# Kernel tuning notes

Measured on AMD Instinct MI355X. Metric: run time of the kernel, lower is better.

## Reference

```python
import jax, jax.numpy as jnp
import numpy as np

N = 100000   # nodes
E = 1000000  # edges (before self-loops)
G = 64       # graphs in batch
IN, HID, OUT = 128, 64, 1


def setup_inputs() -> dict:
    key = jax.random.key(0)
    ks = jax.random.split(key, 24)
    inp = {
        "x": jax.random.normal(ks[0], (N, IN), jnp.float32),
        "adj": jax.random.randint(ks[1], (2, E), 0, N, jnp.int32),
        "batch": jnp.sort(jax.random.randint(ks[2], (N,), 0, G, jnp.int32)),
    }
    i = 3
    dims = [(IN, HID), (HID, HID), (HID, HID)]
    for l, (di, do) in enumerate(dims, start=1):
        inp[f"W{l}"] = jax.random.normal(ks[i], (di, do), jnp.float32) * (1.0 / np.sqrt(di)); i += 1
        inp[f"a_src{l}"] = jax.random.normal(ks[i], (do,), jnp.float32) * 0.1; i += 1
        inp[f"a_dst{l}"] = jax.random.normal(ks[i], (do,), jnp.float32) * 0.1; i += 1
        inp[f"b{l}"] = jnp.zeros((do,), jnp.float32); i += 1
    inp["linnews_W"] = jax.random.normal(ks[i], (IN, HID), jnp.float32) * (1.0 / np.sqrt(IN)); i += 1
    inp["linnews_b"] = jnp.zeros((HID,), jnp.float32)
    inp["lin0_W"] = jax.random.normal(ks[i], (HID, HID), jnp.float32) * (1.0 / np.sqrt(HID)); i += 1
    inp["lin0_b"] = jnp.zeros((HID,), jnp.float32)
    inp["lin1_W"] = jax.random.normal(ks[i], (2 * HID, OUT), jnp.float32) * (1.0 / np.sqrt(2 * HID)); i += 1
    inp["lin1_b"] = jnp.zeros((OUT,), jnp.float32)
    return inp


def _gat_layer(x, src, dst, W, a_src, a_dst, b):
    # PyG GATConv, heads=1, self-loops already appended to (src, dst).
    h = x @ W                                        # [N, HID]
    e = (h @ a_src)[src] + (h @ a_dst)[dst]          # [E'] edge scores
    e = jax.nn.leaky_relu(e, 0.2)
    # segment softmax over incoming edges of each dst node
    m = jax.ops.segment_max(e, dst, num_segments=N)
    num = jnp.exp(e - m[dst])
    den = jax.ops.segment_sum(num, dst, num_segments=N)
    coef = num / (den[dst] + 1e-16)                  # [E']
    out = jax.ops.segment_sum(coef[:, None] * h[src], dst, num_segments=N)
    return out + b


def reference(x, adj, batch, W1, a_src1, a_dst1, b1, W2, a_src2, a_dst2, b2,
              W3, a_src3, a_dst3, b3, linnews_W, linnews_b, lin0_W, lin0_b,
              lin1_W, lin1_b):
    loop = jnp.arange(N, dtype=adj.dtype)
    src = jnp.concatenate([adj[0], loop])
    dst = jnp.concatenate([adj[1], loop])

    h = jax.nn.relu(_gat_layer(x, src, dst, W1, a_src1, a_dst1, b1))
    h = jax.nn.relu(_gat_layer(h, src, dst, W2, a_src2, a_dst2, b2))
    h = jax.nn.relu(_gat_layer(h, src, dst, W3, a_src3, a_dst3, b3))

    # global max pool per graph
    h = jax.ops.segment_max(h, batch, num_segments=G)        # [G, HID]
    h = jax.nn.relu(h @ lin0_W + lin0_b)

    # root node of each graph = first index with that batch id
    root = jax.ops.segment_min(jnp.arange(N), batch, num_segments=G)  # [G]
    news = jax.nn.relu(x[root] @ linnews_W + linnews_b)      # [G, HID]

    out = jnp.concatenate([h, news], axis=-1) @ lin1_W + lin1_b
    return jax.nn.sigmoid(out)                               # [G, 1]
```

## Files before the change

kernel.cpp:

```cpp
#include <hip/hip_runtime.h>
#include <hip/hip_fp16.h>
#include <cstdint>

#define THREADS 256
#define NBLK 64
#define BPAD 512
#define LINBLK 640

typedef _Float16 half8 __attribute__((ext_vector_type(8)));
typedef float v4f __attribute__((ext_vector_type(4)));

__global__ void init_kernel(float* pool, int* root, int G) {
  int i = blockIdx.x * blockDim.x + threadIdx.x;
  if (i < G * 64) pool[i] = 0.0f;
  if (i < G) root[i] = 0x7fffffff;
}

__global__ __launch_bounds__(256) void hist_kernel(const int* __restrict__ dst_e,
                                                   int* __restrict__ hist, int E, int chunk) {
  __shared__ int hcnt[BPAD];
  int t = threadIdx.x, blk = blockIdx.x;
  for (int i = t; i < BPAD; i += 256) hcnt[i] = 0;
  __syncthreads();
  int s = blk * chunk, e = s + chunk;
  if (e > E) e = E;
  for (int i = s + t; i < e; i += 256) atomicAdd(&hcnt[dst_e[i] >> 8], 1);
  __syncthreads();
  for (int b = t; b < BPAD; b += 256) hist[b * NBLK + blk] = hcnt[b];
}

__global__ __launch_bounds__(256) void hscan_kernel(int* __restrict__ hist) {
  __shared__ int part[256];
  const int PER = (BPAD * NBLK) / 256;
  int t = threadIdx.x;
  int base = t * PER;
  int sum = 0;
  for (int k = 0; k < PER; k++) sum += hist[base + k];
  part[t] = sum;
  __syncthreads();
  int own = sum;
  for (int off = 1; off < 256; off <<= 1) {
    int v = (t >= off) ? part[t - off] : 0;
    __syncthreads();
    part[t] += v;
    __syncthreads();
  }
  int run = part[t] - own;
  for (int k = 0; k < PER; k++) {
    int h = hist[base + k];
    hist[base + k] = run;
    run += h;
  }
}

__global__ __launch_bounds__(256) void scatter_kernel(const int* __restrict__ src_e,
                                                      const int* __restrict__ dst_e,
                                                      const int* __restrict__ hist,
                                                      unsigned int* __restrict__ ebuf,
                                                      int E, int chunk) {
  __shared__ int cur[BPAD];
  int t = threadIdx.x, blk = blockIdx.x;
  for (int b = t; b < BPAD; b += 256) cur[b] = hist[b * NBLK + blk];
  __syncthreads();
  int s = blk * chunk, e = s + chunk;
  if (e > E) e = E;
  for (int i = s + t; i < e; i += 256) {
    int d = dst_e[i];
    unsigned int sv = (unsigned int)src_e[i];
    int slot = atomicAdd(&cur[d >> 8], 1);
    ebuf[slot] = (sv << 8) | (unsigned int)(d & 255);
  }
}

__global__ __launch_bounds__(256) void build_kernel(const unsigned int* __restrict__ ebuf,
                                                    const int* __restrict__ hist,
                                                    int* __restrict__ row_start,
                                                    int* __restrict__ csr_src,
                                                    unsigned char* __restrict__ dst8,
                                                    int N, int E) {
  __shared__ int counts[256];
  __shared__ int sc[256];
  __shared__ int curw[256];
  int t = threadIdx.x, b = blockIdx.x;
  int nbase = b * 256;
  int ebase = hist[b * NBLK];
  int eend = hist[(b + 1) * NBLK];
  counts[t] = 0;
  __syncthreads();
  int ecount = eend - ebase;
  for (int i = t; i < ecount; i += 256)
    atomicAdd(&counts[ebuf[ebase + i] & 255u], 1);
  __syncthreads();
  int n = nbase + t;
  int val = (n < N) ? counts[t] + 1 : 0;
  sc[t] = val;
  __syncthreads();
  int own = val;
  for (int off = 1; off < 256; off <<= 1) {
    int v = (t >= off) ? sc[t - off] : 0;
    __syncthreads();
    sc[t] += v;
    __syncthreads();
  }
  int myloc = sc[t] - own;
  int rowb = ebase + nbase;
  if (n < N) {
    row_start[n] = rowb + myloc;
    csr_src[rowb + myloc + counts[t]] = n;
    dst8[rowb + myloc + counts[t]] = (unsigned char)t;
    if (n == N - 1) row_start[N] = rowb + myloc + counts[t] + 1;
  }
  curw[t] = rowb + myloc;
  __syncthreads();
  for (int i = t; i < ecount; i += 256) {
    unsigned int ev = ebuf[ebase + i];
    int ld = (int)(ev & 255u);
    int pos = atomicAdd(&curw[ld], 1);
    csr_src[pos] = (int)(ev >> 8);
    dst8[pos] = (unsigned char)ld;
  }
}

template <int K>
__global__ __launch_bounds__(256) void lin_attn_kernel(
    const float* __restrict__ in, const float* __restrict__ W,
    const float* __restrict__ a_src, const float* __restrict__ a_dst,
    __half2* __restrict__ h2, float* __restrict__ as_, float* __restrict__ ad_,
    int N, int nwaves) {
  constexpr int NKC = K / 32;
  __shared__ _Float16 sh[4][16 * 64];
  const int t = threadIdx.x;
  const int lane = t & 63, w = t >> 6;
  const int col = lane & 15, quad = lane >> 4;
  const int wid = blockIdx.x * 4 + w;

  half8 bf[4][NKC];
#pragma unroll
  for (int nt = 0; nt < 4; nt++)
#pragma unroll
    for (int kc = 0; kc < NKC; kc++) {
      half8 v;
#pragma unroll
      for (int j = 0; j < 8; j++)
        v[j] = (_Float16)W[(kc * 32 + quad * 8 + j) * 64 + nt * 16 + col];
      bf[nt][kc] = v;
    }
  float sa[4], sd[4];
#pragma unroll
  for (int nt = 0; nt < 4; nt++) {
    sa[nt] = a_src[nt * 16 + col];
    sd[nt] = a_dst[nt * 16 + col];
  }

  const int ntiles = (N + 15) >> 4;
  for (int tile = wid; tile < ntiles; tile += nwaves) {
    const int nb = tile << 4;
    int nodeA = nb + col;
    if (nodeA >= N) nodeA = N - 1;
    const float* arow = in + (size_t)nodeA * K + quad * 8;

    v4f acc[4];
#pragma unroll
    for (int nt = 0; nt < 4; nt++) acc[nt] = (v4f){0.f, 0.f, 0.f, 0.f};

#pragma unroll
    for (int kc = 0; kc < NKC; kc++) {
      float4 f0 = *(const float4*)(arow + kc * 32);
      float4 f1 = *(const float4*)(arow + kc * 32 + 4);
      half8 a;
      a[0] = (_Float16)f0.x; a[1] = (_Float16)f0.y;
      a[2] = (_Float16)f0.z; a[3] = (_Float16)f0.w;
      a[4] = (_Float16)f1.x; a[5] = (_Float16)f1.y;
      a[6] = (_Float16)f1.z; a[7] = (_Float16)f1.w;
#pragma unroll
      for (int nt = 0; nt < 4; nt++)
        acc[nt] = __builtin_amdgcn_mfma_f32_16x16x32_f16(a, bf[nt][kc], acc[nt], 0, 0, 0);
    }

    float ps[4], pd[4];
#pragma unroll
    for (int r = 0; r < 4; r++) { ps[r] = 0.f; pd[r] = 0.f; }
#pragma unroll
    for (int nt = 0; nt < 4; nt++)
#pragma unroll
      for (int r = 0; r < 4; r++) {
        ps[r] += acc[nt][r] * sa[nt];
        pd[r] += acc[nt][r] * sd[nt];
      }
#pragma unroll
    for (int r = 0; r < 4; r++)
#pragma unroll
      for (int m = 1; m < 16; m <<= 1) {
        ps[r] += __shfl_xor(ps[r], m);
        pd[r] += __shfl_xor(pd[r], m);
      }
    if (col == 0) {
#pragma unroll
      for (int r = 0; r < 4; r++) {
        int node = nb + quad * 4 + r;
        if (node < N) { as_[node] = ps[r]; ad_[node] = pd[r]; }
      }
    }

#pragma unroll
    for (int nt = 0; nt < 4; nt++)
#pragma unroll
      for (int r = 0; r < 4; r++)
        sh[w][(quad * 4 + r) * 64 + nt * 16 + col] = (_Float16)acc[nt][r];
    int nr = lane >> 2, c4 = lane & 3;
    float4 v0 = *(float4*)&sh[w][nr * 64 + c4 * 16];
    float4 v1 = *(float4*)&sh[w][nr * 64 + c4 * 16 + 8];
    int node = nb + nr;
    if (node < N) {
      *(float4*)&h2[(size_t)node * 32 + c4 * 8] = v0;
      *(float4*)&h2[(size_t)node * 32 + c4 * 8 + 4] = v1;
    }
  }
}

__global__ __launch_bounds__(256) void score_kernel(
    const float* __restrict__ as_, const float* __restrict__ ad_,
    const int* __restrict__ csr_src, const unsigned char* __restrict__ dst8,
    const int* __restrict__ row_start, float* __restrict__ coef, int N) {
  int b = blockIdx.x;
  int part = blockIdx.y;
  int nbase = b * 256;
  int nend = nbase + 256; if (nend > N) nend = N;
  int sBeg = row_start[nbase];
  int sEnd = row_start[nend];
  for (int s = sBeg + part * 256 + threadIdx.x; s < sEnd; s += 1024) {
    int src = csr_src[s];
    float e = as_[src] + ad_[nbase + dst8[s]];
    e = (e > 0.f) ? e : 0.2f * e;
    coef[s] = __expf(e);
  }
}

__global__ __launch_bounds__(256) void agg_kernel(
    const __half2* __restrict__ h2, const float* __restrict__ coef,
    const int* __restrict__ csr_src, const int* __restrict__ row_start,
    const float* __restrict__ b, float* __restrict__ out, int N) {
  int t = threadIdx.x;
  int lane = t & 63, w = t >> 6;
  int ng = lane >> 3, co = lane & 7;
  int n = blockIdx.x * 32 + w * 8 + ng;
  if (n >= N) return;
  int rs = row_start[n], re = row_start[n + 1];
  const float4* h4 = (const float4*)h2;

  float4 A0 = make_float4(0.f, 0.f, 0.f, 0.f);
  float4 A1 = make_float4(0.f, 0.f, 0.f, 0.f);
  float den = 0.f;
  for (int s = rs; s < re; s += 4) {
    float cf[4];
    int src[4];
#pragma unroll
    for (int j = 0; j < 4; j++) {
      int sj = s + j;
      int sc = (sj < re) ? sj : (re - 1);
      cf[j] = coef[sc];
      if (sj >= re) cf[j] = 0.f;
      src[j] = csr_src[sc];
    }
#pragma unroll
    for (int j = 0; j < 4; j++) {
      float4 hv = h4[(size_t)src[j] * 8 + co];
      const __half2* hp = (const __half2*)&hv;
      float2 f0 = __half22float2(hp[0]);
      float2 f1 = __half22float2(hp[1]);
      float2 f2 = __half22float2(hp[2]);
      float2 f3 = __half22float2(hp[3]);
      float c = cf[j];
      den += c;
      A0.x += c * f0.x; A0.y += c * f0.y; A0.z += c * f1.x; A0.w += c * f1.y;
      A1.x += c * f2.x; A1.y += c * f2.y; A1.z += c * f3.x; A1.w += c * f3.y;
    }
  }
  float inv = 1.0f / (den + 1e-16f);
  float4 b0 = *(const float4*)&b[co * 8];
  float4 b1 = *(const float4*)&b[co * 8 + 4];
  float4 o0, o1;
  o0.x = fmaxf(A0.x * inv + b0.x, 0.f);
  o0.y = fmaxf(A0.y * inv + b0.y, 0.f);
  o0.z = fmaxf(A0.z * inv + b0.z, 0.f);
  o0.w = fmaxf(A0.w * inv + b0.w, 0.f);
  o1.x = fmaxf(A1.x * inv + b1.x, 0.f);
  o1.y = fmaxf(A1.y * inv + b1.y, 0.f);
  o1.z = fmaxf(A1.z * inv + b1.z, 0.f);
  o1.w = fmaxf(A1.w * inv + b1.w, 0.f);
  *(float4*)&out[(size_t)n * 64 + co * 8] = o0;
  *(float4*)&out[(size_t)n * 64 + co * 8 + 4] = o1;
}

__global__ void pool_kernel(const float* __restrict__ h, const int* __restrict__ batch,
                            float* __restrict__ pool, int* __restrict__ root,
                            int N, int chunk) {
  int t = threadIdx.x;
  int lane = t & 63, w = t >> 6;
  int row = blockIdx.x * 4 + w;
  int start = row * chunk;
  if (start >= N) return;
  int end = start + chunk; if (end > N) end = N;
  int cur_g = batch[start];
  if (lane == 0 && (start == 0 || batch[start - 1] != cur_g)) atomicMin(&root[cur_g], start);
  float rm = 0.0f;
  for (int n = start; n < end; n++) {
    int g = batch[n];
    if (g != cur_g) {
      atomicMax((int*)&pool[(size_t)cur_g * 64 + lane], __float_as_int(rm));
      if (lane == 0) atomicMin(&root[g], n);
      cur_g = g;
      rm = 0.0f;
    }
    rm = fmaxf(rm, h[(size_t)n * 64 + lane]);
  }
  atomicMax((int*)&pool[(size_t)cur_g * 64 + lane], __float_as_int(rm));
}

__global__ void final_kernel(const float* __restrict__ pool, const int* __restrict__ root,
                             const float* __restrict__ x,
                             const float* __restrict__ lin0_W, const float* __restrict__ lin0_b,
                             const float* __restrict__ linnews_W, const float* __restrict__ linnews_b,
                             const float* __restrict__ lin1_W, const float* __restrict__ lin1_b,
                             float* __restrict__ out, int G, int N) {
  int t = threadIdx.x;
  int lane = t & 63, w = t >> 6;
  int g = blockIdx.x * 4 + w;
  if (g >= G) return;
  float hp = 0.f;
  for (int k = 0; k < 64; k++) hp += pool[(size_t)g * 64 + k] * lin0_W[k * 64 + lane];
  hp = fmaxf(hp + lin0_b[lane], 0.f);
  int r = root[g]; if (r > N - 1) r = N - 1; if (r < 0) r = 0;
  float nw = 0.f;
  for (int k = 0; k < 128; k++) nw += x[(size_t)r * 128 + k] * linnews_W[k * 64 + lane];
  nw = fmaxf(nw + linnews_b[lane], 0.f);
  float p = hp * lin1_W[lane] + nw * lin1_W[64 + lane];
  for (int k = 1; k < 64; k <<= 1) p += __shfl_xor(p, k);
  if (lane == 0) out[g] = 1.0f / (1.0f + __expf(-(p + lin1_b[0])));
}

extern "C" void kernel_launch(void* const* d_in, const int* in_sizes, int n_in,
                              void* d_out, int out_size, void* d_ws, size_t ws_size,
                              hipStream_t stream) {
  (void)n_in; (void)ws_size;
  const float* x      = (const float*)d_in[0];
  const int*   adj    = (const int*)d_in[1];
  const int*   batch  = (const int*)d_in[2];
  const float* W1     = (const float*)d_in[3];
  const float* asrc1  = (const float*)d_in[4];
  const float* adst1  = (const float*)d_in[5];
  const float* b1     = (const float*)d_in[6];
  const float* W2     = (const float*)d_in[7];
  const float* asrc2  = (const float*)d_in[8];
  const float* adst2  = (const float*)d_in[9];
  const float* b2     = (const float*)d_in[10];
  const float* W3     = (const float*)d_in[11];
  const float* asrc3  = (const float*)d_in[12];
  const float* adst3  = (const float*)d_in[13];
  const float* b3     = (const float*)d_in[14];
  const float* lnW    = (const float*)d_in[15];
  const float* lnb    = (const float*)d_in[16];
  const float* l0W    = (const float*)d_in[17];
  const float* l0b    = (const float*)d_in[18];
  const float* l1W    = (const float*)d_in[19];
  const float* l1b    = (const float*)d_in[20];
  float* outp = (float*)d_out;

  const int N = in_sizes[2];
  const int E = in_sizes[1] / 2;
  const int Etot = E + N;
  const int G = out_size;
  const int B = (N + 255) / 256;

  const int* src_e = adj;
  const int* dst_e = adj + E;

  uintptr_t p = (uintptr_t)d_ws;
  auto alloc = [&](size_t bytes) -> void* {
    void* r = (void*)p;
    p += (bytes + 255) & ~(size_t)255;
    return r;
  };
  int*     hist      = (int*)alloc((size_t)BPAD * NBLK * 4);
  int*     row_start = (int*)alloc((size_t)(N + 1) * 4);
  int*     csr_src   = (int*)alloc((size_t)Etot * 4);
  unsigned char* dst8 = (unsigned char*)alloc((size_t)Etot);
  float*   coef      = (float*)alloc((size_t)Etot * 4);
  unsigned int* ebuf = (unsigned int*)alloc((size_t)E * 4);
  __half2* h2        = (__half2*)alloc((size_t)N * 32 * 4);
  float*   bufA      = (float*)alloc((size_t)N * 64 * 4);
  float*   as_       = (float*)alloc((size_t)N * 4);
  float*   ad_       = (float*)alloc((size_t)N * 4);
  float*   pool      = (float*)alloc((size_t)G * 64 * 4);
  int*     root      = (int*)alloc((size_t)G * 4);

  init_kernel<<<dim3((G * 64 + THREADS - 1) / THREADS), dim3(THREADS), 0, stream>>>(pool, root, G);

  int chunk = (E + NBLK - 1) / NBLK;
  hist_kernel<<<dim3(NBLK), dim3(256), 0, stream>>>(dst_e, hist, E, chunk);
  hscan_kernel<<<dim3(1), dim3(256), 0, stream>>>(hist);
  scatter_kernel<<<dim3(NBLK), dim3(256), 0, stream>>>(src_e, dst_e, hist, ebuf, E, chunk);
  build_kernel<<<dim3(B), dim3(256), 0, stream>>>(ebuf, hist, row_start, csr_src, dst8, N, E);

  const int aggGrid = (N + 31) / 32;
  const int nwaves = LINBLK * 4;
  dim3 scoreGrid(B, 4);

  lin_attn_kernel<128><<<dim3(LINBLK), dim3(256), 0, stream>>>(x, W1, asrc1, adst1, h2, as_, ad_, N, nwaves);
  score_kernel<<<scoreGrid, dim3(256), 0, stream>>>(as_, ad_, csr_src, dst8, row_start, coef, N);
  agg_kernel<<<dim3(aggGrid), dim3(256), 0, stream>>>(h2, coef, csr_src, row_start, b1, bufA, N);
  lin_attn_kernel<64><<<dim3(LINBLK), dim3(256), 0, stream>>>(bufA, W2, asrc2, adst2, h2, as_, ad_, N, nwaves);
  score_kernel<<<scoreGrid, dim3(256), 0, stream>>>(as_, ad_, csr_src, dst8, row_start, coef, N);
  agg_kernel<<<dim3(aggGrid), dim3(256), 0, stream>>>(h2, coef, csr_src, row_start, b2, bufA, N);
  lin_attn_kernel<64><<<dim3(LINBLK), dim3(256), 0, stream>>>(bufA, W3, asrc3, adst3, h2, as_, ad_, N, nwaves);
  score_kernel<<<scoreGrid, dim3(256), 0, stream>>>(as_, ad_, csr_src, dst8, row_start, coef, N);
  agg_kernel<<<dim3(aggGrid), dim3(256), 0, stream>>>(h2, coef, csr_src, row_start, b3, bufA, N);

  const int ROWS = 2048;
  int pchunk = (N + ROWS - 1) / ROWS;
  pool_kernel<<<dim3(ROWS / 4), dim3(256), 0, stream>>>(bufA, batch, pool, root, N, pchunk);

  final_kernel<<<dim3((G + 3) / 4), dim3(256), 0, stream>>>(
      pool, root, x, l0W, l0b, lnW, lnb, l1W, l1b, outp, G, N);
}
```

Baseline: 358.3 us.

## Fuse edge scoring into aggregation, store layer outputs in fp16, merge init

```diff
diff --git a/kernel.cpp b/kernel.cpp
--- a/kernel.cpp
+++ b/kernel.cpp
@@ -1,6 +1,7 @@
 #include <hip/hip_runtime.h>
 #include <hip/hip_fp16.h>
 #include <cstdint>
+#include <type_traits>
 
 #define THREADS 256
 #define NBLK 64
@@ -10,16 +11,16 @@
 typedef _Float16 half8 __attribute__((ext_vector_type(8)));
 typedef float v4f __attribute__((ext_vector_type(4)));
 
-__global__ void init_kernel(float* pool, int* root, int G) {
-  int i = blockIdx.x * blockDim.x + threadIdx.x;
-  if (i < G * 64) pool[i] = 0.0f;
-  if (i < G) root[i] = 0x7fffffff;
-}
-
 __global__ __launch_bounds__(256) void hist_kernel(const int* __restrict__ dst_e,
-                                                   int* __restrict__ hist, int E, int chunk) {
+                                                   int* __restrict__ hist, int E, int chunk,
+                                                   float* __restrict__ pool, int* __restrict__ root,
+                                                   int G) {
   __shared__ int hcnt[BPAD];
   int t = threadIdx.x, blk = blockIdx.x;
+  if (blk == 0) {
+    for (int i = t; i < G * 64; i += 256) pool[i] = 0.0f;
+    for (int i = t; i < G; i += 256) root[i] = 0x7fffffff;
+  }
   for (int i = t; i < BPAD; i += 256) hcnt[i] = 0;
   __syncthreads();
   int s = blk * chunk, e = s + chunk;
@@ -76,7 +77,6 @@
                                                     const int* __restrict__ hist,
                                                     int* __restrict__ row_start,
                                                     int* __restrict__ csr_src,
-                                                    unsigned char* __restrict__ dst8,
                                                     int N, int E) {
   __shared__ int counts[256];
   __shared__ int sc[256];
@@ -107,23 +107,20 @@
   if (n < N) {
     row_start[n] = rowb + myloc;
     csr_src[rowb + myloc + counts[t]] = n;
-    dst8[rowb + myloc + counts[t]] = (unsigned char)t;
     if (n == N - 1) row_start[N] = rowb + myloc + counts[t] + 1;
   }
   curw[t] = rowb + myloc;
   __syncthreads();
   for (int i = t; i < ecount; i += 256) {
     unsigned int ev = ebuf[ebase + i];
-    int ld = (int)(ev & 255u);
-    int pos = atomicAdd(&curw[ld], 1);
+    int pos = atomicAdd(&curw[ev & 255u], 1);
     csr_src[pos] = (int)(ev >> 8);
-    dst8[pos] = (unsigned char)ld;
-  }
-}
-
-template <int K>
+  }
+}
+
+template <int K, typename TIN>
 __global__ __launch_bounds__(256) void lin_attn_kernel(
-    const float* __restrict__ in, const float* __restrict__ W,
+    const TIN* __restrict__ in, const float* __restrict__ W,
     const float* __restrict__ a_src, const float* __restrict__ a_dst,
     __half2* __restrict__ h2, float* __restrict__ as_, float* __restrict__ ad_,
     int N, int nwaves) {
@@ -157,7 +154,7 @@
     const int nb = tile << 4;
     int nodeA = nb + col;
     if (nodeA >= N) nodeA = N - 1;
-    const float* arow = in + (size_t)nodeA * K + quad * 8;
+    const TIN* arow = in + (size_t)nodeA * K + quad * 8;
 
     v4f acc[4];
 #pragma unroll
@@ -165,13 +162,17 @@
 
 #pragma unroll
     for (int kc = 0; kc < NKC; kc++) {
-      float4 f0 = *(const float4*)(arow + kc * 32);
-      float4 f1 = *(const float4*)(arow + kc * 32 + 4);
       half8 a;
-      a[0] = (_Float16)f0.x; a[1] = (_Float16)f0.y;
-      a[2] = (_Float16)f0.z; a[3] = (_Float16)f0.w;
-      a[4] = (_Float16)f1.x; a[5] = (_Float16)f1.y;
-      a[6] = (_Float16)f1.z; a[7] = (_Float16)f1.w;
+      if constexpr (std::is_same<TIN, float>::value) {
+        float4 f0 = *(const float4*)(arow + kc * 32);
+        float4 f1 = *(const float4*)(arow + kc * 32 + 4);
+        a[0] = (_Float16)f0.x; a[1] = (_Float16)f0.y;
+        a[2] = (_Float16)f0.z; a[3] = (_Float16)f0.w;
+        a[4] = (_Float16)f1.x; a[5] = (_Float16)f1.y;
+        a[6] = (_Float16)f1.z; a[7] = (_Float16)f1.w;
+      } else {
+        a = *(const half8*)(arow + kc * 32);
+      }
 #pragma unroll
       for (int nt = 0; nt < 4; nt++)
         acc[nt] = __builtin_amdgcn_mfma_f32_16x16x32_f16(a, bf[nt][kc], acc[nt], 0, 0, 0);
@@ -218,49 +219,35 @@
   }
 }
 
-__global__ __launch_bounds__(256) void score_kernel(
-    const float* __restrict__ as_, const float* __restrict__ ad_,
-    const int* __restrict__ csr_src, const unsigned char* __restrict__ dst8,
-    const int* __restrict__ row_start, float* __restrict__ coef, int N) {
-  int b = blockIdx.x;
-  int part = blockIdx.y;
-  int nbase = b * 256;
-  int nend = nbase + 256; if (nend > N) nend = N;
-  int sBeg = row_start[nbase];
-  int sEnd = row_start[nend];
-  for (int s = sBeg + part * 256 + threadIdx.x; s < sEnd; s += 1024) {
-    int src = csr_src[s];
-    float e = as_[src] + ad_[nbase + dst8[s]];
-    e = (e > 0.f) ? e : 0.2f * e;
-    coef[s] = __expf(e);
-  }
-}
-
 __global__ __launch_bounds__(256) void agg_kernel(
-    const __half2* __restrict__ h2, const float* __restrict__ coef,
+    const __half2* __restrict__ h2, const float* __restrict__ as_, const float* __restrict__ ad_,
     const int* __restrict__ csr_src, const int* __restrict__ row_start,
-    const float* __restrict__ b, float* __restrict__ out, int N) {
+    const float* __restrict__ b, _Float16* __restrict__ out16, int N) {
   int t = threadIdx.x;
   int lane = t & 63, w = t >> 6;
   int ng = lane >> 3, co = lane & 7;
   int n = blockIdx.x * 32 + w * 8 + ng;
   if (n >= N) return;
   int rs = row_start[n], re = row_start[n + 1];
+  float adn = ad_[n];
   const float4* h4 = (const float4*)h2;
 
   float4 A0 = make_float4(0.f, 0.f, 0.f, 0.f);
   float4 A1 = make_float4(0.f, 0.f, 0.f, 0.f);
   float den = 0.f;
   for (int s = rs; s < re; s += 4) {
-    float cf[4];
     int src[4];
 #pragma unroll
     for (int j = 0; j < 4; j++) {
       int sj = s + j;
-      int sc = (sj < re) ? sj : (re - 1);
-      cf[j] = coef[sc];
-      if (sj >= re) cf[j] = 0.f;
-      src[j] = csr_src[sc];
+      src[j] = csr_src[(sj < re) ? sj : (re - 1)];
+    }
+    float cf[4];
+#pragma unroll
+    for (int j = 0; j < 4; j++) {
+      float e = as_[src[j]] + adn;
+      e = fmaxf(e, 0.2f * e);
+      cf[j] = (s + j < re) ? __expf(e) : 0.f;
     }
 #pragma unroll
     for (int j = 0; j < 4; j++) {
@@ -279,20 +266,19 @@
   float inv = 1.0f / (den + 1e-16f);
   float4 b0 = *(const float4*)&b[co * 8];
   float4 b1 = *(const float4*)&b[co * 8 + 4];
-  float4 o0, o1;
-  o0.x = fmaxf(A0.x * inv + b0.x, 0.f);
-  o0.y = fmaxf(A0.y * inv + b0.y, 0.f);
-  o0.z = fmaxf(A0.z * inv + b0.z, 0.f);
-  o0.w = fmaxf(A0.w * inv + b0.w, 0.f);
-  o1.x = fmaxf(A1.x * inv + b1.x, 0.f);
-  o1.y = fmaxf(A1.y * inv + b1.y, 0.f);
-  o1.z = fmaxf(A1.z * inv + b1.z, 0.f);
-  o1.w = fmaxf(A1.w * inv + b1.w, 0.f);
-  *(float4*)&out[(size_t)n * 64 + co * 8] = o0;
-  *(float4*)&out[(size_t)n * 64 + co * 8 + 4] = o1;
-}
-
-__global__ void pool_kernel(const float* __restrict__ h, const int* __restrict__ batch,
+  _Float16 o[8];
+  o[0] = (_Float16)fmaxf(A0.x * inv + b0.x, 0.f);
+  o[1] = (_Float16)fmaxf(A0.y * inv + b0.y, 0.f);
+  o[2] = (_Float16)fmaxf(A0.z * inv + b0.z, 0.f);
+  o[3] = (_Float16)fmaxf(A0.w * inv + b0.w, 0.f);
+  o[4] = (_Float16)fmaxf(A1.x * inv + b1.x, 0.f);
+  o[5] = (_Float16)fmaxf(A1.y * inv + b1.y, 0.f);
+  o[6] = (_Float16)fmaxf(A1.z * inv + b1.z, 0.f);
+  o[7] = (_Float16)fmaxf(A1.w * inv + b1.w, 0.f);
+  *(float4*)&out16[(size_t)n * 64 + co * 8] = *(float4*)o;
+}
+
+__global__ void pool_kernel(const _Float16* __restrict__ h, const int* __restrict__ batch,
                             float* __restrict__ pool, int* __restrict__ root,
                             int N, int chunk) {
   int t = threadIdx.x;
@@ -312,7 +298,7 @@
       cur_g = g;
       rm = 0.0f;
     }
-    rm = fmaxf(rm, h[(size_t)n * 64 + lane]);
+    rm = fmaxf(rm, (float)h[(size_t)n * 64 + lane]);
   }
   atomicMax((int*)&pool[(size_t)cur_g * 64 + lane], __float_as_int(rm));
 }
@@ -381,44 +367,39 @@
     p += (bytes + 255) & ~(size_t)255;
     return r;
   };
-  int*     hist      = (int*)alloc((size_t)BPAD * NBLK * 4);
-  int*     row_start = (int*)alloc((size_t)(N + 1) * 4);
-  int*     csr_src   = (int*)alloc((size_t)Etot * 4);
-  unsigned char* dst8 = (unsigned char*)alloc((size_t)Etot);
-  float*   coef      = (float*)alloc((size_t)Etot * 4);
-  unsigned int* ebuf = (unsigned int*)alloc((size_t)E * 4);
-  __half2* h2        = (__half2*)alloc((size_t)N * 32 * 4);
-  float*   bufA      = (float*)alloc((size_t)N * 64 * 4);
-  float*   as_       = (float*)alloc((size_t)N * 4);
-  float*   ad_       = (float*)alloc((size_t)N * 4);
-  float*   pool      = (float*)alloc((size_t)G * 64 * 4);
-  int*     root      = (int*)alloc((size_t)G * 4);
-
-  init_kernel<<<dim3((G * 64 + THREADS - 1) / THREADS), dim3(THREADS), 0, stream>>>(pool, root, G);
+  int*      hist      = (int*)alloc((size_t)BPAD * NBLK * 4);
+  int*      row_start = (int*)alloc((size_t)(N + 1) * 4);
+  int*      csr_src   = (int*)alloc((size_t)Etot * 4);
+  unsigned int* ebuf  = (unsigned int*)alloc((size_t)E * 4);
+  __half2*  hbufL     = (__half2*)alloc((size_t)N * 32 * 4);
+  _Float16* hbufA     = (_Float16*)alloc((size_t)N * 64 * 2);
+  float*    as_       = (float*)alloc((size_t)N * 4);
+  float*    ad_       = (float*)alloc((size_t)N * 4);
+  float*    pool      = (float*)alloc((size_t)G * 64 * 4);
+  int*      root      = (int*)alloc((size_t)G * 4);
 
   int chunk = (E + NBLK - 1) / NBLK;
-  hist_kernel<<<dim3(NBLK), dim3(256), 0, stream>>>(dst_e, hist, E, chunk);
+  hist_kernel<<<dim3(NBLK), dim3(256), 0, stream>>>(dst_e, hist, E, chunk, pool, root, G);
   hscan_kernel<<<dim3(1), dim3(256), 0, stream>>>(hist);
   scatter_kernel<<<dim3(NBLK), dim3(256), 0, stream>>>(src_e, dst_e, hist, ebuf, E, chunk);
-  build_kernel<<<dim3(B), dim3(256), 0, stream>>>(ebuf, hist, row_start, csr_src, dst8, N, E);
+  build_kernel<<<dim3(B), dim3(256), 0, stream>>>(ebuf, hist, row_start, csr_src, N, E);
 
   const int aggGrid = (N + 31) / 32;
   const int nwaves = LINBLK * 4;
-  dim3 scoreGrid(B, 4);
-
-  lin_attn_kernel<128><<<dim3(LINBLK), dim3(256), 0, stream>>>(x, W1, asrc1, adst1, h2, as_, ad_, N, nwaves);
-  score_kernel<<<scoreGrid, dim3(256), 0, stream>>>(as_, ad_, csr_src, dst8, row_start, coef, N);
-  agg_kernel<<<dim3(aggGrid), dim3(256), 0, stream>>>(h2, coef, csr_src, row_start, b1, bufA, N);
-  lin_attn_kernel<64><<<dim3(LINBLK), dim3(256), 0, stream>>>(bufA, W2, asrc2, adst2, h2, as_, ad_, N, nwaves);
-  score_kernel<<<scoreGrid, dim3(256), 0, stream>>>(as_, ad_, csr_src, dst8, row_start, coef, N);
-  agg_kernel<<<dim3(aggGrid), dim3(256), 0, stream>>>(h2, coef, csr_src, row_start, b2, bufA, N);
-  lin_attn_kernel<64><<<dim3(LINBLK), dim3(256), 0, stream>>>(bufA, W3, asrc3, adst3, h2, as_, ad_, N, nwaves);
-  score_kernel<<<scoreGrid, dim3(256), 0, stream>>>(as_, ad_, csr_src, dst8, row_start, coef, N);
-  agg_kernel<<<dim3(aggGrid), dim3(256), 0, stream>>>(h2, coef, csr_src, row_start, b3, bufA, N);
+
+  lin_attn_kernel<128, float><<<dim3(LINBLK), dim3(256), 0, stream>>>(
+      x, W1, asrc1, adst1, hbufL, as_, ad_, N, nwaves);
+  agg_kernel<<<dim3(aggGrid), dim3(256), 0, stream>>>(hbufL, as_, ad_, csr_src, row_start, b1, hbufA, N);
+  lin_attn_kernel<64, _Float16><<<dim3(LINBLK), dim3(256), 0, stream>>>(
+      hbufA, W2, asrc2, adst2, hbufL, as_, ad_, N, nwaves);
+  agg_kernel<<<dim3(aggGrid), dim3(256), 0, stream>>>(hbufL, as_, ad_, csr_src, row_start, b2, hbufA, N);
+  lin_attn_kernel<64, _Float16><<<dim3(LINBLK), dim3(256), 0, stream>>>(
+      hbufA, W3, asrc3, adst3, hbufL, as_, ad_, N, nwaves);
+  agg_kernel<<<dim3(aggGrid), dim3(256), 0, stream>>>(hbufL, as_, ad_, csr_src, row_start, b3, hbufA, N);
 
   const int ROWS = 2048;
   int pchunk = (N + ROWS - 1) / ROWS;
-  pool_kernel<<<dim3(ROWS / 4), dim3(256), 0, stream>>>(bufA, batch, pool, root, N, pchunk);
+  pool_kernel<<<dim3(ROWS / 4), dim3(256), 0, stream>>>(hbufA, batch, pool, root, N, pchunk);
 
   final_kernel<<<dim3((G + 3) / 4), dim3(256), 0, stream>>>(
       pool, root, x, l0W, l0b, lnW, lnb, l1W, l1b, outp, G, N);
```

Result: faster. 319.7 us (median of 2 runs) (-10.8%).
